# Optimization experiments

Hardware: AMD Instinct MI355X
Metric: run time of the kernel (lower is better)

The kernel has to match this reference:

```python
import jax, jax.numpy as jnp
import numpy as np

IC = 196        # number of input channels / recurrence steps
B, N = 32, 8192 # batch, points per batch


def setup_inputs() -> dict:
    key = jax.random.key(0)
    ks = jax.random.split(key, 9)
    n = IC - 1  # 195 ReLU cells
    # stacked weights for the 195 distinct rnn cells: Linear(2,6)->ReLU->Linear(6,1)->ReLU
    W1 = jax.random.normal(ks[0], (n, 2, 6), dtype=jnp.float32) * (1.0 / np.sqrt(2.0))
    b1 = jax.random.normal(ks[1], (n, 6), dtype=jnp.float32) * 0.05
    W2 = jax.random.normal(ks[2], (n, 6, 1), dtype=jnp.float32) * (1.0 / np.sqrt(6.0))
    b2 = jax.random.normal(ks[3], (n, 1), dtype=jnp.float32) * 0.05
    # final sigmoid cell: Linear(2,6)->ReLU->Linear(6,1)->Sigmoid
    Wf1 = jax.random.normal(ks[4], (2, 6), dtype=jnp.float32) * (1.0 / np.sqrt(2.0))
    bf1 = jax.random.normal(ks[5], (6,), dtype=jnp.float32) * 0.05
    Wf2 = jax.random.normal(ks[6], (6, 1), dtype=jnp.float32) * (1.0 / np.sqrt(6.0))
    bf2 = jax.random.normal(ks[7], (1,), dtype=jnp.float32) * 0.05
    x = jax.random.normal(ks[8], (B, N, IC), dtype=jnp.float32)
    return {"x": x, "W1": W1, "b1": b1, "W2": W2, "b2": b2,
            "Wf1": Wf1, "bf1": bf1, "Wf2": Wf2, "bf2": bf2}


def reference(x, W1, b1, W2, b2, Wf1, bf1, Wf2, bf2):
    # x: [B, N, IC]. Recurrence: y0 = x[..., 0:1]; for i in 0..IC-2:
    #   y = relu_cell_i(concat(x[..., i:i+1], y));  final: sigmoid cell on x[..., IC-1].
    xs = jnp.moveaxis(x, -1, 0)          # [IC, B, N]
    y0 = xs[0][..., None]                # [B, N, 1]

    def step(y, inp):
        xi, w1, bb1, w2, bb2 = inp
        z = jnp.concatenate([xi[..., None], y], axis=-1)        # [B, N, 2]
        h = jax.nn.relu(jnp.einsum('bni,io->bno', z, w1) + bb1)  # [B, N, 6]
        y = jax.nn.relu(jnp.einsum('bnh,ho->bno', h, w2) + bb2)  # [B, N, 1]
        return y, None

    y, _ = jax.lax.scan(step, y0, (xs[:IC - 1], W1, b1, W2, b2))
    zf = jnp.concatenate([xs[IC - 1][..., None], y], axis=-1)    # [B, N, 2]
    hf = jax.nn.relu(jnp.einsum('bni,io->bno', zf, Wf1) + bf1)
    return jax.nn.sigmoid(jnp.einsum('bnh,ho->bno', hf, Wf2) + bf2)  # [B, N, 1]
```

## Files before the change

kernel.cpp:

```cpp
#include <hip/hip_runtime.h>
#include <math.h>

#define ICC 196
#define CH  16
#define NPH 12
#define RS  260
#define BLK 256

#define PINV(x) asm volatile("" : "+v"(x))
#define PINS(x) asm volatile("" : "+s"(x))

struct Wc {
    float a0,a1,a2,a3,a4,a5,a6,a7,a8,a9,a10,a11;
    float c0,c1,c2,c3,c4,c5;
    float d0,d1,d2,d3,d4,d5;
    float e0;
};

__device__ __forceinline__ Wc loadW(int i,
    const float* __restrict__ W1, const float* __restrict__ b1,
    const float* __restrict__ W2, const float* __restrict__ b2)
{
    Wc w;
    const float* p = W1 + i * 12;
    w.a0=p[0]; w.a1=p[1]; w.a2=p[2];  w.a3=p[3];  w.a4=p[4];  w.a5=p[5];
    w.a6=p[6]; w.a7=p[7]; w.a8=p[8];  w.a9=p[9];  w.a10=p[10]; w.a11=p[11];
    const float* q = b1 + i * 6;
    w.c0=q[0]; w.c1=q[1]; w.c2=q[2]; w.c3=q[3]; w.c4=q[4]; w.c5=q[5];
    const float* r = W2 + i * 6;
    w.d0=r[0]; w.d1=r[1]; w.d2=r[2]; w.d3=r[3]; w.d4=r[4]; w.d5=r[5];
    w.e0 = b2[i];
    return w;
}

__device__ __forceinline__ void pinW(Wc& w) {
    PINS(w.a0); PINS(w.a1); PINS(w.a2);  PINS(w.a3);  PINS(w.a4);  PINS(w.a5);
    PINS(w.a6); PINS(w.a7); PINS(w.a8);  PINS(w.a9);  PINS(w.a10); PINS(w.a11);
    PINS(w.c0); PINS(w.c1); PINS(w.c2);  PINS(w.c3);  PINS(w.c4);  PINS(w.c5);
    PINS(w.d0); PINS(w.d1); PINS(w.d2);  PINS(w.d3);  PINS(w.d4);  PINS(w.d5);
    PINS(w.e0);
}

__device__ __forceinline__ float cellW(float xi, float y, const Wc& w)
{
    float h0 = fmaxf(fmaf(y, w.a6,  fmaf(xi, w.a0, w.c0)), 0.0f);
    float h1 = fmaxf(fmaf(y, w.a7,  fmaf(xi, w.a1, w.c1)), 0.0f);
    float h2 = fmaxf(fmaf(y, w.a8,  fmaf(xi, w.a2, w.c2)), 0.0f);
    float h3 = fmaxf(fmaf(y, w.a9,  fmaf(xi, w.a3, w.c3)), 0.0f);
    float h4 = fmaxf(fmaf(y, w.a10, fmaf(xi, w.a4, w.c4)), 0.0f);
    float h5 = fmaxf(fmaf(y, w.a11, fmaf(xi, w.a5, w.c5)), 0.0f);
    float s0 = fmaf(h0, w.d0, fmaf(h1, w.d1, w.e0));
    float s1 = fmaf(h2, w.d2, h3 * w.d3);
    float s2 = fmaf(h4, w.d4, h5 * w.d5);
    return fmaxf(s0 + (s1 + s2), 0.0f);
}

__global__ __launch_bounds__(BLK, 4) void rnn_kernel(
    const float* __restrict__ x,
    const float* __restrict__ W1,
    const float* __restrict__ b1,
    const float* __restrict__ W2,
    const float* __restrict__ b2,
    const float* __restrict__ Wf1,
    const float* __restrict__ bf1,
    const float* __restrict__ Wf2,
    const float* __restrict__ bf2,
    float* __restrict__ out,
    int npoints)
{
    __shared__ float tile[CH * RS];

    const int tid = threadIdx.x;
    const int p0  = blockIdx.x * BLK;
    const int p   = p0 + tid;

    const int rl0 = tid >> 2;
    const int q4  = (tid & 3) * 4;

    float4 rA[4];

    const int pc_self = (p < npoints) ? p : (npoints - 1);
    const float4 tail = *reinterpret_cast<const float4*>(
        x + (size_t)pc_self * ICC + 192);

    #pragma unroll
    for (int k = 0; k < 4; ++k) {
        int rl = rl0 + 64 * k;
        int pc = p0 + rl; if (pc >= npoints) pc = npoints - 1;
        rA[k] = *reinterpret_cast<const float4*>(x + (size_t)pc * ICC + 0 * CH + q4);
    }
    #pragma unroll
    for (int k = 0; k < 4; ++k) {
        int rl = rl0 + 64 * k;
        tile[(q4 + 0) * RS + rl] = rA[k].x;
        tile[(q4 + 1) * RS + rl] = rA[k].y;
        tile[(q4 + 2) * RS + rl] = rA[k].z;
        tile[(q4 + 3) * RS + rl] = rA[k].w;
    }
    #pragma unroll
    for (int k = 0; k < 4; ++k) {
        int rl = rl0 + 64 * k;
        int pc = p0 + rl; if (pc >= npoints) pc = npoints - 1;
        rA[k] = *reinterpret_cast<const float4*>(x + (size_t)pc * ICC + 1 * CH + q4);
    }
    __syncthreads();

    float y = tile[0 * RS + tid];

    #pragma unroll 1
    for (int c = 0; c < NPH; ++c) {
        Wc wc = loadW(c * CH, W1, b1, W2, b2);

        float xi[CH];
        #pragma unroll
        for (int j = 0; j < CH; ++j)
            xi[j] = tile[j * RS + tid];
        #pragma unroll
        for (int j = 0; j < CH; ++j)
            PINV(xi[j]);

        pinW(wc);

        if (c < NPH - 1) {
            __syncthreads();
            #pragma unroll
            for (int k = 0; k < 4; ++k) {
                int rl = rl0 + 64 * k;
                tile[(q4 + 0) * RS + rl] = rA[k].x;
                tile[(q4 + 1) * RS + rl] = rA[k].y;
                tile[(q4 + 2) * RS + rl] = rA[k].z;
                tile[(q4 + 3) * RS + rl] = rA[k].w;
            }
            if (c < NPH - 2) {
                #pragma unroll
                for (int k = 0; k < 4; ++k) {
                    int rl = rl0 + 64 * k;
                    int pc = p0 + rl; if (pc >= npoints) pc = npoints - 1;
                    rA[k] = *reinterpret_cast<const float4*>(
                        x + (size_t)pc * ICC + (c + 2) * CH + q4);
                }
            }
            __syncthreads();
        }

        #pragma unroll
        for (int j = 0; j < CH; ++j) {
            Wc wn;
            if (j < CH - 1) wn = loadW(c * CH + j + 1, W1, b1, W2, b2);
            y = cellW(xi[j], y, wc);
            if (j < CH - 1) { pinW(wn); wc = wn; }
        }
    }

    {
        Wc w192 = loadW(192, W1, b1, W2, b2);
        Wc w193 = loadW(193, W1, b1, W2, b2);
        Wc w194 = loadW(194, W1, b1, W2, b2);
        y = cellW(tail.x, y, w192);
        y = cellW(tail.y, y, w193);
        y = cellW(tail.z, y, w194);
    }

    const float xf = tail.w;
    float h0 = fmaxf(fmaf(y, Wf1[6],  fmaf(xf, Wf1[0], bf1[0])), 0.0f);
    float h1 = fmaxf(fmaf(y, Wf1[7],  fmaf(xf, Wf1[1], bf1[1])), 0.0f);
    float h2 = fmaxf(fmaf(y, Wf1[8],  fmaf(xf, Wf1[2], bf1[2])), 0.0f);
    float h3 = fmaxf(fmaf(y, Wf1[9],  fmaf(xf, Wf1[3], bf1[3])), 0.0f);
    float h4 = fmaxf(fmaf(y, Wf1[10], fmaf(xf, Wf1[4], bf1[4])), 0.0f);
    float h5 = fmaxf(fmaf(y, Wf1[11], fmaf(xf, Wf1[5], bf1[5])), 0.0f);
    float s0 = fmaf(h0, Wf2[0], fmaf(h1, Wf2[1], bf2[0]));
    float s1 = fmaf(h2, Wf2[2], h3 * Wf2[3]);
    float s2 = fmaf(h4, Wf2[4], h5 * Wf2[5]);
    float t  = s0 + (s1 + s2);

    if (p < npoints)
        out[p] = 1.0f / (1.0f + __expf(-t));
}

extern "C" void kernel_launch(void* const* d_in, const int* in_sizes, int n_in,
                              void* d_out, int out_size, void* d_ws, size_t ws_size,
                              hipStream_t stream) {
    const float* x   = (const float*)d_in[0];
    const float* W1  = (const float*)d_in[1];
    const float* b1  = (const float*)d_in[2];
    const float* W2  = (const float*)d_in[3];
    const float* b2  = (const float*)d_in[4];
    const float* Wf1 = (const float*)d_in[5];
    const float* bf1 = (const float*)d_in[6];
    const float* Wf2 = (const float*)d_in[7];
    const float* bf2 = (const float*)d_in[8];
    float* out = (float*)d_out;

    const int npoints = out_size;
    const int grid = (npoints + BLK - 1) / BLK;
    rnn_kernel<<<grid, BLK, 0, stream>>>(x, W1, b1, W2, b2,
                                         Wf1, bf1, Wf2, bf2, out, npoints);
}
```

Measured before the change: 88.87 us.

## Double-buffer LDS tiles with point-major layout and manual waitcnt pipelining

```diff
diff --git a/kernel.cpp b/kernel.cpp
--- a/kernel.cpp
+++ b/kernel.cpp
@@ -4,11 +4,16 @@
 #define ICC 196
 #define CH  16
 #define NPH 12
-#define RS  260
+#define RS2 20
 #define BLK 256
 
-#define PINV(x) asm volatile("" : "+v"(x))
-#define PINS(x) asm volatile("" : "+s"(x))
+#define PINV(v)  asm volatile("" : "+v"(v))
+#define PINS(v)  asm volatile("" : "+s"(v))
+#define WAIT_VM4 asm volatile("s_waitcnt vmcnt(4)" ::: "memory")
+#define WAIT_VM0 asm volatile("s_waitcnt vmcnt(0)" ::: "memory")
+#define WAIT_LG0 asm volatile("s_waitcnt lgkmcnt(0)" ::: "memory")
+#define SFENCE   __builtin_amdgcn_sched_barrier(0)
+#define SBAR     __builtin_amdgcn_s_barrier()
 
 struct Wc {
     float a0,a1,a2,a3,a4,a5,a6,a7,a8,a9,a10,a11;
@@ -55,6 +60,45 @@
     return fmaxf(s0 + (s1 + s2), 0.0f);
 }
 
+#define RNN_PHASE(CC, BUF, WCUR, WNXT, DO_ISSUE, DO_VM4, DO_WRITE)            \
+  {                                                                           \
+    const float* tb = &tile[BUF][tid * RS2];                                  \
+    float4 xa = *reinterpret_cast<const float4*>(tb + 0);                     \
+    float4 xb = *reinterpret_cast<const float4*>(tb + 4);                     \
+    float4 xc = *reinterpret_cast<const float4*>(tb + 8);                     \
+    float4 xd = *reinterpret_cast<const float4*>(tb + 12);                    \
+    Wc wc = loadW((CC) * CH, W1, b1, W2, b2);                                 \
+    if (DO_ISSUE) {                                                           \
+      WNXT[0] = *reinterpret_cast<const float4*>(bp0 + (size_t)((CC)+2)*CH);  \
+      WNXT[1] = *reinterpret_cast<const float4*>(bp1 + (size_t)((CC)+2)*CH);  \
+      WNXT[2] = *reinterpret_cast<const float4*>(bp2 + (size_t)((CC)+2)*CH);  \
+      WNXT[3] = *reinterpret_cast<const float4*>(bp3 + (size_t)((CC)+2)*CH);  \
+    }                                                                         \
+    SFENCE;                                                                   \
+    if (DO_WRITE) {                                                           \
+      if (DO_VM4) { WAIT_VM4; } else { WAIT_VM0; }                            \
+      SFENCE;                                                                 \
+      float* tw = &tile[1 - (BUF)][rl0 * RS2 + cq];                           \
+      *reinterpret_cast<float4*>(tw + 0 * 64 * RS2) = WCUR[0];                \
+      *reinterpret_cast<float4*>(tw + 1 * 64 * RS2) = WCUR[1];                \
+      *reinterpret_cast<float4*>(tw + 2 * 64 * RS2) = WCUR[2];                \
+      *reinterpret_cast<float4*>(tw + 3 * 64 * RS2) = WCUR[3];                \
+    }                                                                         \
+    float xi[CH] = { xa.x, xa.y, xa.z, xa.w, xb.x, xb.y, xb.z, xb.w,          \
+                     xc.x, xc.y, xc.z, xc.w, xd.x, xd.y, xd.z, xd.w };        \
+    _Pragma("unroll")                                                         \
+    for (int j = 0; j < CH; ++j) PINV(xi[j]);                                 \
+    pinW(wc);                                                                 \
+    _Pragma("unroll")                                                         \
+    for (int j = 0; j < CH; ++j) {                                            \
+      Wc wn;                                                                  \
+      if (j < CH - 1) wn = loadW((CC) * CH + j + 1, W1, b1, W2, b2);          \
+      y = cellW(xi[j], y, wc);                                                \
+      if (j < CH - 1) { pinW(wn); wc = wn; }                                  \
+    }                                                                         \
+    if (DO_WRITE) { WAIT_LG0; SBAR; }                                         \
+  }
+
 __global__ __launch_bounds__(BLK, 4) void rnn_kernel(
     const float* __restrict__ x,
     const float* __restrict__ W1,
@@ -68,90 +112,58 @@
     float* __restrict__ out,
     int npoints)
 {
-    __shared__ float tile[CH * RS];
+    __shared__ float tile[2][BLK * RS2];
 
     const int tid = threadIdx.x;
     const int p0  = blockIdx.x * BLK;
     const int p   = p0 + tid;
 
     const int rl0 = tid >> 2;
-    const int q4  = (tid & 3) * 4;
-
-    float4 rA[4];
+    const int cq  = (tid & 3) * 4;
+
+    int pr0 = p0 + rl0 +   0; if (pr0 >= npoints) pr0 = npoints - 1;
+    int pr1 = p0 + rl0 +  64; if (pr1 >= npoints) pr1 = npoints - 1;
+    int pr2 = p0 + rl0 + 128; if (pr2 >= npoints) pr2 = npoints - 1;
+    int pr3 = p0 + rl0 + 192; if (pr3 >= npoints) pr3 = npoints - 1;
+    const float* bp0 = x + (size_t)pr0 * ICC + cq;
+    const float* bp1 = x + (size_t)pr1 * ICC + cq;
+    const float* bp2 = x + (size_t)pr2 * ICC + cq;
+    const float* bp3 = x + (size_t)pr3 * ICC + cq;
+
+    float4 rA[4], rB[4];
+
+    rA[0] = *reinterpret_cast<const float4*>(bp0);
+    rA[1] = *reinterpret_cast<const float4*>(bp1);
+    rA[2] = *reinterpret_cast<const float4*>(bp2);
+    rA[3] = *reinterpret_cast<const float4*>(bp3);
+    rB[0] = *reinterpret_cast<const float4*>(bp0 + CH);
+    rB[1] = *reinterpret_cast<const float4*>(bp1 + CH);
+    rB[2] = *reinterpret_cast<const float4*>(bp2 + CH);
+    rB[3] = *reinterpret_cast<const float4*>(bp3 + CH);
+    SFENCE;
+    WAIT_VM4; SFENCE;
+    {
+        float* tw = &tile[0][rl0 * RS2 + cq];
+        *reinterpret_cast<float4*>(tw + 0 * 64 * RS2) = rA[0];
+        *reinterpret_cast<float4*>(tw + 1 * 64 * RS2) = rA[1];
+        *reinterpret_cast<float4*>(tw + 2 * 64 * RS2) = rA[2];
+        *reinterpret_cast<float4*>(tw + 3 * 64 * RS2) = rA[3];
+    }
+    WAIT_LG0; SBAR;
+
+    float y = tile[0][tid * RS2];
+
+    #pragma unroll 1
+    for (int c2 = 0; c2 < NPH - 2; c2 += 2) {
+        RNN_PHASE(c2,     0, rB, rA, 1, 1, 1);
+        RNN_PHASE(c2 + 1, 1, rA, rB, 1, 1, 1);
+    }
+    RNN_PHASE(10, 0, rB, rA, 0, 0, 1);
+    RNN_PHASE(11, 1, rA, rB, 0, 0, 0);
 
     const int pc_self = (p < npoints) ? p : (npoints - 1);
     const float4 tail = *reinterpret_cast<const float4*>(
         x + (size_t)pc_self * ICC + 192);
-
-    #pragma unroll
-    for (int k = 0; k < 4; ++k) {
-        int rl = rl0 + 64 * k;
-        int pc = p0 + rl; if (pc >= npoints) pc = npoints - 1;
-        rA[k] = *reinterpret_cast<const float4*>(x + (size_t)pc * ICC + 0 * CH + q4);
-    }
-    #pragma unroll
-    for (int k = 0; k < 4; ++k) {
-        int rl = rl0 + 64 * k;
-        tile[(q4 + 0) * RS + rl] = rA[k].x;
-        tile[(q4 + 1) * RS + rl] = rA[k].y;
-        tile[(q4 + 2) * RS + rl] = rA[k].z;
-        tile[(q4 + 3) * RS + rl] = rA[k].w;
-    }
-    #pragma unroll
-    for (int k = 0; k < 4; ++k) {
-        int rl = rl0 + 64 * k;
-        int pc = p0 + rl; if (pc >= npoints) pc = npoints - 1;
-        rA[k] = *reinterpret_cast<const float4*>(x + (size_t)pc * ICC + 1 * CH + q4);
-    }
-    __syncthreads();
-
-    float y = tile[0 * RS + tid];
-
-    #pragma unroll 1
-    for (int c = 0; c < NPH; ++c) {
-        Wc wc = loadW(c * CH, W1, b1, W2, b2);
-
-        float xi[CH];
-        #pragma unroll
-        for (int j = 0; j < CH; ++j)
-            xi[j] = tile[j * RS + tid];
-        #pragma unroll
-        for (int j = 0; j < CH; ++j)
-            PINV(xi[j]);
-
-        pinW(wc);
-
-        if (c < NPH - 1) {
-            __syncthreads();
-            #pragma unroll
-            for (int k = 0; k < 4; ++k) {
-                int rl = rl0 + 64 * k;
-                tile[(q4 + 0) * RS + rl] = rA[k].x;
-                tile[(q4 + 1) * RS + rl] = rA[k].y;
-                tile[(q4 + 2) * RS + rl] = rA[k].z;
-                tile[(q4 + 3) * RS + rl] = rA[k].w;
-            }
-            if (c < NPH - 2) {
-                #pragma unroll
-                for (int k = 0; k < 4; ++k) {
-                    int rl = rl0 + 64 * k;
-                    int pc = p0 + rl; if (pc >= npoints) pc = npoints - 1;
-                    rA[k] = *reinterpret_cast<const float4*>(
-                        x + (size_t)pc * ICC + (c + 2) * CH + q4);
-                }
-            }
-            __syncthreads();
-        }
-
-        #pragma unroll
-        for (int j = 0; j < CH; ++j) {
-            Wc wn;
-            if (j < CH - 1) wn = loadW(c * CH + j + 1, W1, b1, W2, b2);
-            y = cellW(xi[j], y, wc);
-            if (j < CH - 1) { pinW(wn); wc = wn; }
-        }
-    }
-
     {
         Wc w192 = loadW(192, W1, b1, W2, b2);
         Wc w193 = loadW(193, W1, b1, W2, b2);
```

After: 157.5 us. 1.77x slower.

## Drop LDS transpose; load per-thread rows directly into registers with double buffering

Applied to the files above, without the earlier changes.

```diff
diff --git a/kernel.cpp b/kernel.cpp
--- a/kernel.cpp
+++ b/kernel.cpp
@@ -2,13 +2,10 @@
 #include <math.h>
 
 #define ICC 196
-#define CH  16
-#define NPH 12
-#define RS  260
 #define BLK 256
 
-#define PINV(x) asm volatile("" : "+v"(x))
-#define PINS(x) asm volatile("" : "+s"(x))
+#define PINS(v)  asm volatile("" : "+s"(v))
+#define SFENCE   __builtin_amdgcn_sched_barrier(0)
 
 struct Wc {
     float a0,a1,a2,a3,a4,a5,a6,a7,a8,a9,a10,a11;
@@ -55,6 +52,29 @@
     return fmaxf(s0 + (s1 + s2), 0.0f);
 }
 
+#define BURST16(CB, X0, X1, X2, X3)                                           \
+  {                                                                           \
+    Wc wc = loadW((CB), W1, b1, W2, b2);                                      \
+    pinW(wc);                                                                 \
+    Wc wn;                                                                    \
+    wn = loadW((CB)+1,  W1,b1,W2,b2); y = cellW(X0.x, y, wc); pinW(wn); wc = wn; \
+    wn = loadW((CB)+2,  W1,b1,W2,b2); y = cellW(X0.y, y, wc); pinW(wn); wc = wn; \
+    wn = loadW((CB)+3,  W1,b1,W2,b2); y = cellW(X0.z, y, wc); pinW(wn); wc = wn; \
+    wn = loadW((CB)+4,  W1,b1,W2,b2); y = cellW(X0.w, y, wc); pinW(wn); wc = wn; \
+    wn = loadW((CB)+5,  W1,b1,W2,b2); y = cellW(X1.x, y, wc); pinW(wn); wc = wn; \
+    wn = loadW((CB)+6,  W1,b1,W2,b2); y = cellW(X1.y, y, wc); pinW(wn); wc = wn; \
+    wn = loadW((CB)+7,  W1,b1,W2,b2); y = cellW(X1.z, y, wc); pinW(wn); wc = wn; \
+    wn = loadW((CB)+8,  W1,b1,W2,b2); y = cellW(X1.w, y, wc); pinW(wn); wc = wn; \
+    wn = loadW((CB)+9,  W1,b1,W2,b2); y = cellW(X2.x, y, wc); pinW(wn); wc = wn; \
+    wn = loadW((CB)+10, W1,b1,W2,b2); y = cellW(X2.y, y, wc); pinW(wn); wc = wn; \
+    wn = loadW((CB)+11, W1,b1,W2,b2); y = cellW(X2.z, y, wc); pinW(wn); wc = wn; \
+    wn = loadW((CB)+12, W1,b1,W2,b2); y = cellW(X2.w, y, wc); pinW(wn); wc = wn; \
+    wn = loadW((CB)+13, W1,b1,W2,b2); y = cellW(X3.x, y, wc); pinW(wn); wc = wn; \
+    wn = loadW((CB)+14, W1,b1,W2,b2); y = cellW(X3.y, y, wc); pinW(wn); wc = wn; \
+    wn = loadW((CB)+15, W1,b1,W2,b2); y = cellW(X3.z, y, wc); pinW(wn); wc = wn; \
+    y = cellW(X3.w, y, wc);                                                   \
+  }
+
 __global__ __launch_bounds__(BLK, 4) void rnn_kernel(
     const float* __restrict__ x,
     const float* __restrict__ W1,
@@ -68,87 +88,33 @@
     float* __restrict__ out,
     int npoints)
 {
-    __shared__ float tile[CH * RS];
+    const int tid = threadIdx.x;
+    const int p   = blockIdx.x * BLK + tid;
+    const int pc  = (p < npoints) ? p : (npoints - 1);
+    const float4* __restrict__ r4 =
+        reinterpret_cast<const float4*>(x + (size_t)pc * ICC);
 
-    const int tid = threadIdx.x;
-    const int p0  = blockIdx.x * BLK;
-    const int p   = p0 + tid;
+    float4 A0,A1,A2,A3, B0,B1,B2,B3, T;
+    A0 = r4[0]; A1 = r4[1]; A2 = r4[2]; A3 = r4[3];
+    B0 = r4[4]; B1 = r4[5]; B2 = r4[6]; B3 = r4[7];
+    T  = r4[48];
+    SFENCE;
 
-    const int rl0 = tid >> 2;
-    const int q4  = (tid & 3) * 4;
-
-    float4 rA[4];
-
-    const int pc_self = (p < npoints) ? p : (npoints - 1);
-    const float4 tail = *reinterpret_cast<const float4*>(
-        x + (size_t)pc_self * ICC + 192);
-
-    #pragma unroll
-    for (int k = 0; k < 4; ++k) {
-        int rl = rl0 + 64 * k;
-        int pc = p0 + rl; if (pc >= npoints) pc = npoints - 1;
-        rA[k] = *reinterpret_cast<const float4*>(x + (size_t)pc * ICC + 0 * CH + q4);
-    }
-    #pragma unroll
-    for (int k = 0; k < 4; ++k) {
-        int rl = rl0 + 64 * k;
-        tile[(q4 + 0) * RS + rl] = rA[k].x;
-        tile[(q4 + 1) * RS + rl] = rA[k].y;
-        tile[(q4 + 2) * RS + rl] = rA[k].z;
-        tile[(q4 + 3) * RS + rl] = rA[k].w;
-    }
-    #pragma unroll
-    for (int k = 0; k < 4; ++k) {
-        int rl = rl0 + 64 * k;
-        int pc = p0 + rl; if (pc >= npoints) pc = npoints - 1;
-        rA[k] = *reinterpret_cast<const float4*>(x + (size_t)pc * ICC + 1 * CH + q4);
-    }
-    __syncthreads();
-
-    float y = tile[0 * RS + tid];
+    float y = A0.x;
 
     #pragma unroll 1
-    for (int c = 0; c < NPH; ++c) {
-        Wc wc = loadW(c * CH, W1, b1, W2, b2);
-
-        float xi[CH];
-        #pragma unroll
-        for (int j = 0; j < CH; ++j)
-            xi[j] = tile[j * RS + tid];
-        #pragma unroll
-        for (int j = 0; j < CH; ++j)
-            PINV(xi[j]);
-
-        pinW(wc);
-
-        if (c < NPH - 1) {
-            __syncthreads();
-            #pragma unroll
-            for (int k = 0; k < 4; ++k) {
-                int rl = rl0 + 64 * k;
-                tile[(q4 + 0) * RS + rl] = rA[k].x;
-                tile[(q4 + 1) * RS + rl] = rA[k].y;
-                tile[(q4 + 2) * RS + rl] = rA[k].z;
-                tile[(q4 + 3) * RS + rl] = rA[k].w;
-            }
-            if (c < NPH - 2) {
-                #pragma unroll
-                for (int k = 0; k < 4; ++k) {
-                    int rl = rl0 + 64 * k;
-                    int pc = p0 + rl; if (pc >= npoints) pc = npoints - 1;
-                    rA[k] = *reinterpret_cast<const float4*>(
-                        x + (size_t)pc * ICC + (c + 2) * CH + q4);
-                }
-            }
-            __syncthreads();
+    for (int c2 = 0; c2 < 12; c2 += 2) {
+        BURST16(c2 * 16, A0, A1, A2, A3);
+        if (c2 < 10) {
+            const float4* q = r4 + (c2 + 2) * 4;
+            A0 = q[0]; A1 = q[1]; A2 = q[2]; A3 = q[3];
+            SFENCE;
         }
-
-        #pragma unroll
-        for (int j = 0; j < CH; ++j) {
-            Wc wn;
-            if (j < CH - 1) wn = loadW(c * CH + j + 1, W1, b1, W2, b2);
-            y = cellW(xi[j], y, wc);
-            if (j < CH - 1) { pinW(wn); wc = wn; }
+        BURST16(c2 * 16 + 16, B0, B1, B2, B3);
+        if (c2 < 10) {
+            const float4* q = r4 + (c2 + 3) * 4;
+            B0 = q[0]; B1 = q[1]; B2 = q[2]; B3 = q[3];
+            SFENCE;
         }
     }
 
@@ -156,12 +122,12 @@
         Wc w192 = loadW(192, W1, b1, W2, b2);
         Wc w193 = loadW(193, W1, b1, W2, b2);
         Wc w194 = loadW(194, W1, b1, W2, b2);
-        y = cellW(tail.x, y, w192);
-        y = cellW(tail.y, y, w193);
-        y = cellW(tail.z, y, w194);
+        y = cellW(T.x, y, w192);
+        y = cellW(T.y, y, w193);
+        y = cellW(T.z, y, w194);
     }
 
-    const float xf = tail.w;
+    const float xf = T.w;
     float h0 = fmaxf(fmaf(y, Wf1[6],  fmaf(xf, Wf1[0], bf1[0])), 0.0f);
     float h1 = fmaxf(fmaf(y, Wf1[7],  fmaf(xf, Wf1[1], bf1[1])), 0.0f);
     float h2 = fmaxf(fmaf(y, Wf1[8],  fmaf(xf, Wf1[2], bf1[2])), 0.0f);
```

New measurement: 153.0 us. +72.1%, slower.
